# Performance work log

Measured on AMD Instinct MI355X. Metric: run time of the kernel, lower is better.

## Reference

```python
import jax, jax.numpy as jnp
import numpy as np

B, T, C, H = 4, 2048, 1024, 16
D = C // H  # head dim = 64


def setup_inputs() -> dict:
    key = jax.random.key(0)
    ks = jax.random.split(key, 5)
    s = 1.0 / np.sqrt(C)
    return {
        "x": jax.random.normal(ks[0], (B, T, C), jnp.float32),
        "Wq": jax.random.normal(ks[1], (C, C), jnp.float32) * s,
        "bq": jnp.zeros((C,), jnp.float32),
        "Wk": jax.random.normal(ks[2], (C, C), jnp.float32) * s,
        "bk": jnp.zeros((C,), jnp.float32),
        "Wv": jax.random.normal(ks[3], (C, C), jnp.float32) * s,
        "bv": jnp.zeros((C,), jnp.float32),
        "Wp": jax.random.normal(ks[4], (C, C), jnp.float32) * s,
        "bp": jnp.zeros((C,), jnp.float32),
    }


def reference(x, Wq, bq, Wk, bk, Wv, bv, Wp, bp):
    # linear projections -> [B, H, T, D]
    def heads(t):
        return t.reshape(B, T, H, D).transpose(0, 2, 1, 3)
    q = heads(x @ Wq.T + bq)
    k = heads(x @ Wk.T + bk)
    v = heads(x @ Wv.T + bv)
    scale = 1.0 / np.sqrt(D)
    att = jnp.einsum("bhtd,bhsd->bhts", q, k) * scale  # [B,H,T,T]
    causal = jnp.tril(jnp.ones((T, T), bool))
    att = jnp.where(causal[None, None], att, -jnp.inf)
    att = jax.nn.softmax(att, axis=-1)
    y = jnp.einsum("bhts,bhsd->bhtd", att, v)  # [B,H,T,D]
    y = y.transpose(0, 2, 1, 3).reshape(B, T, C)
    return y @ Wp.T + bp
```

## Files before the change

### kernel.cpp

```cpp
#include <hip/hip_runtime.h>

typedef float f32x4 __attribute__((ext_vector_type(4)));
typedef float f32x16 __attribute__((ext_vector_type(16)));
typedef __bf16 bf16x8 __attribute__((ext_vector_type(8)));
typedef unsigned short u16x8 __attribute__((ext_vector_type(8)));
typedef unsigned int u32x4 __attribute__((ext_vector_type(4)));

#define SCQ 0.1803368801111183f

__device__ inline unsigned short f2bf(float f) {
  unsigned int u = __builtin_bit_cast(unsigned int, f);
  u += 0x7FFFu + ((u >> 16) & 1u);
  return (unsigned short)(u >> 16);
}

__device__ inline float fexp2(float x) {
#if __has_builtin(__builtin_amdgcn_exp2f)
  return __builtin_amdgcn_exp2f(x);
#else
  return exp2f(x);
#endif
}

__device__ inline unsigned int cvtpk_bf16(float a, float b) {
  unsigned int r;
  __asm__("v_cvt_pk_bf16_f32 %0, %1, %2" : "=v"(r) : "v"(a), "v"(b));
  return r;
}
__device__ inline void permswap32(unsigned int& a, unsigned int& b) {
  __asm__("v_permlane32_swap_b32 %0, %1" : "+v"(a), "+v"(b));
}

__device__ inline void gload_lds16(const unsigned short* g, unsigned short* l) {
  __builtin_amdgcn_global_load_lds(
      (const __attribute__((address_space(1))) unsigned int*)g,
      (__attribute__((address_space(3))) unsigned int*)l, 16, 0, 0);
}

__global__ void cvt_x(const float* __restrict__ in, unsigned short* __restrict__ out) {
  int i = (blockIdx.x * 256 + threadIdx.x) * 4;
  float4 f = *(const float4*)(in + i);
  ushort4 o;
  o.x = f2bf(f.x); o.y = f2bf(f.y); o.z = f2bf(f.z); o.w = f2bf(f.w);
  *(ushort4*)(out + i) = o;
}

__global__ void cvt_w(const float* __restrict__ a, const float* __restrict__ b,
                      const float* __restrict__ c, const float* __restrict__ d,
                      unsigned short* __restrict__ oa, unsigned short* __restrict__ ob,
                      unsigned short* __restrict__ oc, unsigned short* __restrict__ od) {
  const float* src[4] = {a, b, c, d};
  unsigned short* dst[4] = {oa, ob, oc, od};
  int m = blockIdx.y;
  int i = (blockIdx.x * 256 + threadIdx.x) * 4;
  float4 f = *(const float4*)(src[m] + i);
  ushort4 o;
  o.x = f2bf(f.x); o.y = f2bf(f.y); o.z = f2bf(f.z); o.w = f2bf(f.w);
  *(ushort4*)(dst[m] + i) = o;
}

template <int MODE>
__global__ __launch_bounds__(512, 2) void gemm256(const unsigned short* __restrict__ A,
                                                  const unsigned short* __restrict__ Bt,
                                                  const float* __restrict__ b0,
                                                  const float* __restrict__ b1,
                                                  const float* __restrict__ b2,
                                                  void* __restrict__ out,
                                                  int M, int N, int K) {
  __shared__ __align__(16) unsigned short Lg[2][4][128 * 64];
  const int tid = threadIdx.x;
  const int lane = tid & 63, w = tid >> 6;
  const int qm = w >> 2, qn = w & 3;
  const int l15 = lane & 15, kq = lane >> 4;

  const int nwg = gridDim.x, qx = nwg >> 3;
  const int wg = blockIdx.x;
  const int wgs = (wg & 7) * qx + (wg >> 3);
  const int nbm = M >> 8;
  const int bm = wgs % nbm, bn = wgs / nbm;
  const int m0 = bm * 256, n0 = bn * 256;
  const int NT = K >> 6, NT4 = NT << 2;

  const int row0 = tid >> 3, c0 = (tid & 7) ^ (row0 & 7);
  const int row1 = row0 + 64, c1 = (tid & 7) ^ (row1 & 7);
  const int ch0 = tid, ch1 = tid + 512;

  auto stage = [&](int g) {
    if (g < NT4) {
      const int tt = g >> 2, h = g & 3;
      const unsigned short* s_;
      int rbase, reg_;
      if (h == 0)      { s_ = A;  rbase = m0;       reg_ = 0; }
      else if (h == 3) { s_ = A;  rbase = m0 + 128; reg_ = 1; }
      else if (h == 1) { s_ = Bt; rbase = n0;       reg_ = 2; }
      else             { s_ = Bt; rbase = n0 + 128; reg_ = 3; }
      unsigned short* d = &Lg[tt & 1][reg_][0];
      gload_lds16(s_ + (size_t)(rbase + row0) * K + tt * 64 + c0 * 8, d + ch0 * 8);
      gload_lds16(s_ + (size_t)(rbase + row1) * K + tt * 64 + c1 * 8, d + ch1 * 8);
    }
  };

  auto rdAh = [&](const unsigned short* R, u16x8 (&a)[4][2]) {
#pragma unroll
    for (int mf = 0; mf < 4; mf++) {
      int row = qm * 64 + mf * 16 + l15;
#pragma unroll
      for (int kf = 0; kf < 2; kf++) {
        int pc = (kf * 4 + kq) ^ (row & 7);
        a[mf][kf] = *(const u16x8*)(R + row * 64 + pc * 8);
      }
    }
  };
  auto rdBh = [&](const unsigned short* R, u16x8 (&bb)[2][2]) {
#pragma unroll
    for (int nf = 0; nf < 2; nf++) {
      int row = qn * 32 + nf * 16 + l15;
#pragma unroll
      for (int kf = 0; kf < 2; kf++) {
        int pc = (kf * 4 + kq) ^ (row & 7);
        bb[nf][kf] = *(const u16x8*)(R + row * 64 + pc * 8);
      }
    }
  };
  auto domfma = [&](u16x8 (&a)[4][2], u16x8 (&bb)[2][2], f32x4 (*ac)[2]) {
#pragma unroll
    for (int mf = 0; mf < 4; mf++)
#pragma unroll
      for (int nf = 0; nf < 2; nf++)
#pragma unroll
        for (int kf = 0; kf < 2; kf++)
          ac[mf][nf] = __builtin_amdgcn_mfma_f32_16x16x32_bf16(
              __builtin_bit_cast(bf16x8, a[mf][kf]),
              __builtin_bit_cast(bf16x8, bb[nf][kf]), ac[mf][nf], 0, 0, 0);
  };

  f32x4 acc[4][4][2] = {};

#pragma unroll
  for (int g = 0; g < 7; ++g) stage(g);
  __asm__ __volatile__("s_waitcnt vmcnt(6)" ::: "memory");
  __builtin_amdgcn_s_barrier();

  for (int tt = 0; tt < NT; ++tt) {
    const unsigned short* A0r = &Lg[tt & 1][0][0];
    const unsigned short* A1r = &Lg[tt & 1][1][0];
    const unsigned short* B0r = &Lg[tt & 1][2][0];
    const unsigned short* B1r = &Lg[tt & 1][3][0];
    const int gb = 7 + 4 * tt;
    u16x8 aA[4][2], bb0[2][2], bb1[2][2];

    rdAh(A0r, aA); rdBh(B0r, bb0);
    stage(gb + 0);
    __builtin_amdgcn_s_barrier();
    __asm__ __volatile__("s_waitcnt lgkmcnt(0)" ::: "memory");
    __builtin_amdgcn_sched_barrier(0);
    __builtin_amdgcn_s_setprio(1);
    domfma(aA, bb0, acc[0]);
    __builtin_amdgcn_s_setprio(0);
    __builtin_amdgcn_s_barrier();

    rdBh(B1r, bb1);
    stage(gb + 1);
    __builtin_amdgcn_s_barrier();
    __asm__ __volatile__("s_waitcnt lgkmcnt(0)" ::: "memory");
    __builtin_amdgcn_sched_barrier(0);
    __builtin_amdgcn_s_setprio(1);
    domfma(aA, bb1, acc[1]);
    __builtin_amdgcn_s_setprio(0);
    __builtin_amdgcn_s_barrier();

    rdAh(A1r, aA);
    stage(gb + 2);
    __builtin_amdgcn_s_barrier();
    __asm__ __volatile__("s_waitcnt lgkmcnt(0)" ::: "memory");
    __builtin_amdgcn_sched_barrier(0);
    __builtin_amdgcn_s_setprio(1);
    domfma(aA, bb0, acc[2]);
    __builtin_amdgcn_s_setprio(0);
    __builtin_amdgcn_s_barrier();

    stage(gb + 3);
    __builtin_amdgcn_s_setprio(1);
    domfma(aA, bb1, acc[3]);
    __builtin_amdgcn_s_setprio(0);
    if (tt < NT - 2) {
      __asm__ __volatile__("s_waitcnt vmcnt(6)" ::: "memory");
    } else if (tt == NT - 2) {
      __asm__ __volatile__("s_waitcnt vmcnt(0)" ::: "memory");
    }
    __builtin_amdgcn_s_barrier();
  }

#pragma unroll
  for (int p = 0; p < 4; p++) {
    const int rb = m0 + (p >> 1) * 128 + qm * 64 + kq * 4;
    const int cb = n0 + (p & 1) * 128 + qn * 32 + l15;
#pragma unroll
    for (int nf = 0; nf < 2; nf++) {
      const int col = cb + nf * 16;
      float bv, sc;
      int which = 0, cl = col;
      if (MODE == 0) {
        which = col >> 10; cl = col & 1023;
        const float* bp = (which == 0) ? b0 : ((which == 1) ? b1 : b2);
        bv = bp[cl];
        sc = (which == 0) ? SCQ : 1.f;
      } else {
        bv = b0[col]; sc = 1.f;
      }
#pragma unroll
      for (int mf = 0; mf < 4; mf++) {
        f32x4 v4 = acc[p][mf][nf];
#pragma unroll
        for (int r = 0; r < 4; r++) {
          int row = rb + mf * 16 + r;
          float v = (v4[r] + bv) * sc;
          if (MODE == 0) {
            int h = cl >> 6, d = cl & 63;
            int b = row >> 11, t = row & 2047;
            ((unsigned short*)out)[(size_t)which * 8388608 +
                                   ((size_t)((b * 16 + h) * 2048 + t)) * 64 + d] = f2bf(v);
          } else {
            ((float*)out)[(size_t)row * N + col] = v;
          }
        }
      }
    }
  }
}

__global__ __launch_bounds__(256) void transpose_v(const unsigned short* __restrict__ V,
                                                   unsigned short* __restrict__ Vt) {
  constexpr int P = 66;
  __shared__ unsigned short L[64 * P];
  const int tid = threadIdx.x;
  const int bh = blockIdx.y;
  const int t0 = blockIdx.x * 64;
  const unsigned short* Vp = V + (size_t)bh * 2048 * 64;
  unsigned short* Op = Vt + (size_t)bh * 64 * 2048;
#pragma unroll
  for (int j = 0; j < 2; j++) {
    int r = (tid >> 3) + j * 32;
    int c = (tid & 7) * 8;
    u16x8 v = *(const u16x8*)(Vp + (size_t)(t0 + r) * 64 + c);
#pragma unroll
    for (int i = 0; i < 4; i++) {
      unsigned int pk = (unsigned int)v[2 * i] | ((unsigned int)v[2 * i + 1] << 16);
      *(unsigned int*)&L[r * P + c + 2 * i] = pk;
    }
  }
  __syncthreads();
#pragma unroll
  for (int j = 0; j < 2; j++) {
    int ch = j * 256 + tid;
    int d = ch >> 3, tc = (ch & 7) * 8;
    u16x8 o;
#pragma unroll
    for (int k = 0; k < 8; k++) o[k] = L[(tc + k) * P + d];
    *(u16x8*)(Op + (size_t)d * 2048 + t0 + tc) = o;
  }
}

__global__ __launch_bounds__(256, 2) void attn_kernel(const unsigned short* __restrict__ Q,
                                                      const unsigned short* __restrict__ Km,
                                                      const unsigned short* __restrict__ Vt,
                                                      unsigned short* __restrict__ Y) {
  constexpr int T = 2048, D = 64;
  __shared__ __align__(16) unsigned short Ks[2][64 * 64];
  __shared__ __align__(16) unsigned short Vs[2][64 * 64];
  const int tid = threadIdx.x;
  const int lane = tid & 63, w = tid >> 6;
  const int l31 = lane & 31, half = lane >> 5;
  const int bh = blockIdx.x;
  const int b = bh >> 4, h = bh & 15;
  const int p = blockIdx.y;
  const unsigned short* Qp = Q + (size_t)bh * T * D;
  const unsigned short* Kp = Km + (size_t)bh * T * D;
  const unsigned short* Vp = Vt + (size_t)bh * D * T;

  const int bch0 = (w * 2) * 64, bch1 = (w * 2 + 1) * 64;
  const int ch0 = bch0 + lane, ch1 = bch1 + lane;
  const int row0 = ch0 >> 3, c0 = (ch0 & 7) ^ (row0 & 7);
  const int row1 = ch1 >> 3, c1 = (ch1 & 7) ^ (row1 & 7);

  for (int phase = 0; phase < 2; ++phase) {
    const int jt = phase ? (63 - (p * 4 + w)) : (p * 4 + w);
    const int qt = jt * 32;
    const int nit = phase ? (32 - 2 * p) : (2 * p + 2);
    const int qg = qt + l31;

    bf16x8 aq[4];
#pragma unroll
    for (int kc = 0; kc < 4; kc++)
      aq[kc] = *(const bf16x8*)(Qp + (size_t)qg * D + kc * 16 + half * 8);
    __asm__ __volatile__("" :: "v"(__builtin_bit_cast(f32x4, aq[0])),
                              "v"(__builtin_bit_cast(f32x4, aq[1])),
                              "v"(__builtin_bit_cast(f32x4, aq[2])),
                              "v"(__builtin_bit_cast(f32x4, aq[3])));

    f32x16 o0 = {}, o1 = {};
    float lsum = 0.f;

    gload_lds16(Kp + (size_t)row0 * 64 + c0 * 8, Ks[0] + bch0 * 8);
    gload_lds16(Kp + (size_t)row1 * 64 + c1 * 8, Ks[0] + bch1 * 8);
    gload_lds16(Vp + (size_t)row0 * T + c0 * 8, Vs[0] + bch0 * 8);
    gload_lds16(Vp + (size_t)row1 * T + c1 * 8, Vs[0] + bch1 * 8);

    int cur = 0;
    for (int it = 0; it < nit; ++it) {
      const int s0 = it * 64;
      if (it + 1 < nit) {
        const int s1 = s0 + 64;
        unsigned short* kd = Ks[cur ^ 1];
        unsigned short* vd = Vs[cur ^ 1];
        gload_lds16(Kp + (size_t)(s1 + row0) * 64 + c0 * 8, kd + bch0 * 8);
        gload_lds16(Kp + (size_t)(s1 + row1) * 64 + c1 * 8, kd + bch1 * 8);
        gload_lds16(Vp + (size_t)row0 * T + s1 + c0 * 8, vd + bch0 * 8);
        gload_lds16(Vp + (size_t)row1 * T + s1 + c1 * 8, vd + bch1 * 8);
        __asm__ __volatile__("s_waitcnt vmcnt(4)" ::: "memory");
      } else {
        __asm__ __volatile__("s_waitcnt vmcnt(0)" ::: "memory");
      }
      __builtin_amdgcn_s_barrier();
      __builtin_amdgcn_sched_barrier(0);

      if (s0 <= qt + 31) {
        const unsigned short* Kb_ = Ks[cur];
        const unsigned short* Vb_ = Vs[cur];

        f32x16 sacc0 = {}, sacc1 = {};
#pragma unroll
        for (int kc = 0; kc < 4; kc++) {
          int kr0 = l31;
          int cc0 = (kc * 2 + half) ^ (kr0 & 7);
          u16x8 k0 = *(const u16x8*)(Kb_ + kr0 * 64 + cc0 * 8);
          sacc0 = __builtin_amdgcn_mfma_f32_32x32x16_bf16(
              __builtin_bit_cast(bf16x8, k0), aq[kc], sacc0, 0, 0, 0);
          int kr1 = 32 + l31;
          int cc1 = (kc * 2 + half) ^ (kr1 & 7);
          u16x8 k1 = *(const u16x8*)(Kb_ + kr1 * 64 + cc1 * 8);
          sacc1 = __builtin_amdgcn_mfma_f32_32x32x16_bf16(
              __builtin_bit_cast(bf16x8, k1), aq[kc], sacc1, 0, 0, 0);
        }

        const bool full = (s0 + 63) <= qt;
        float e0_[16], e1_[16];
        if (full) {
#pragma unroll
          for (int r = 0; r < 16; r++) { e0_[r] = fexp2(sacc0[r]); lsum += e0_[r]; }
#pragma unroll
          for (int r = 0; r < 16; r++) { e1_[r] = fexp2(sacc1[r]); lsum += e1_[r]; }
        } else {
#pragma unroll
          for (int r = 0; r < 16; r++) {
            int sg = s0 + (r & 3) + 8 * (r >> 2) + 4 * half;
            float ex = fexp2(sacc0[r]);
            ex = (sg > qg) ? 0.f : ex;
            e0_[r] = ex; lsum += ex;
          }
#pragma unroll
          for (int r = 0; r < 16; r++) {
            int sg = s0 + 32 + (r & 3) + 8 * (r >> 2) + 4 * half;
            float ex = fexp2(sacc1[r]);
            ex = (sg > qg) ? 0.f : ex;
            e1_[r] = ex; lsum += ex;
          }
        }

        bf16x8 pf[4];
        auto pack2 = [&](const float* e_, int kbase) {
#pragma unroll
          for (int kl = 0; kl < 2; kl++) {
            int base = kl * 8;
            unsigned int a0 = cvtpk_bf16(e_[base + 0], e_[base + 1]);
            unsigned int b0v = cvtpk_bf16(e_[base + 4], e_[base + 5]);
            permswap32(a0, b0v);
            unsigned int a1 = cvtpk_bf16(e_[base + 2], e_[base + 3]);
            unsigned int b1v = cvtpk_bf16(e_[base + 6], e_[base + 7]);
            permswap32(a1, b1v);
            u32x4 t = {a0, a1, b0v, b1v};
            pf[kbase + kl] = __builtin_bit_cast(bf16x8, t);
          }
        };
        pack2(e0_, 0);
        pack2(e1_, 2);

#pragma unroll
        for (int kc = 0; kc < 4; kc++) {
          int vr0 = l31;
          int cc0 = (kc * 2 + half) ^ (vr0 & 7);
          u16x8 v0 = *(const u16x8*)(Vb_ + vr0 * 64 + cc0 * 8);
          o0 = __builtin_amdgcn_mfma_f32_32x32x16_bf16(
              __builtin_bit_cast(bf16x8, v0), pf[kc], o0, 0, 0, 0);
          int vr1 = 32 + l31;
          int cc1 = (kc * 2 + half) ^ (vr1 & 7);
          u16x8 v1 = *(const u16x8*)(Vb_ + vr1 * 64 + cc1 * 8);
          o1 = __builtin_amdgcn_mfma_f32_32x32x16_bf16(
              __builtin_bit_cast(bf16x8, v1), pf[kc], o1, 0, 0, 0);
        }
      }

      __builtin_amdgcn_sched_barrier(0);
      __builtin_amdgcn_s_barrier();
      cur ^= 1;
    }

    float tot = lsum + __shfl_xor(lsum, 32);
    float inv = 1.f / tot;
    unsigned short* Yrow = Y + ((size_t)(b * T + qg)) * 1024 + h * 64;
#pragma unroll
    for (int rp = 0; rp < 8; rp++) {
      int r = rp * 2;
      int d = (r & 3) + 8 * (r >> 2) + 4 * half;
      *(unsigned int*)(Yrow + d)      = cvtpk_bf16(o0[r] * inv, o0[r + 1] * inv);
      *(unsigned int*)(Yrow + 32 + d) = cvtpk_bf16(o1[r] * inv, o1[r + 1] * inv);
    }
  }
}

extern "C" void kernel_launch(void* const* d_in, const int* in_sizes, int n_in,
                              void* d_out, int out_size, void* d_ws, size_t ws_size,
                              hipStream_t stream) {
  const float* x  = (const float*)d_in[0];
  const float* Wq = (const float*)d_in[1];
  const float* bq = (const float*)d_in[2];
  const float* Wk = (const float*)d_in[3];
  const float* bk = (const float*)d_in[4];
  const float* Wv = (const float*)d_in[5];
  const float* bv = (const float*)d_in[6];
  const float* Wp = (const float*)d_in[7];
  const float* bp = (const float*)d_in[8];

  char* ws = (char*)d_ws;
  unsigned short* xb  = (unsigned short*)(ws + 0);
  unsigned short* wqb = (unsigned short*)(ws + 16777216);
  unsigned short* wkb = (unsigned short*)(ws + 18874368);
  unsigned short* wvb = (unsigned short*)(ws + 20971520);
  unsigned short* wpb = (unsigned short*)(ws + 23068672);
  unsigned short* Qb  = (unsigned short*)(ws + 25165824);
  unsigned short* Kb  = (unsigned short*)(ws + 41943040);
  unsigned short* Vb  = (unsigned short*)(ws + 58720256);
  unsigned short* Vtb = xb;
  unsigned short* Yb  = Vb;

  cvt_x<<<8192, 256, 0, stream>>>(x, xb);
  cvt_w<<<dim3(1024, 4), 256, 0, stream>>>(Wq, Wk, Wv, Wp, wqb, wkb, wvb, wpb);

  gemm256<0><<<384, 512, 0, stream>>>(xb, wqb, bq, bk, bv, Qb, 8192, 3072, 1024);

  transpose_v<<<dim3(32, 64), 256, 0, stream>>>(Vb, Vtb);
  attn_kernel<<<dim3(64, 8), 256, 0, stream>>>(Qb, Kb, Vtb, Yb);

  gemm256<1><<<128, 512, 0, stream>>>(Yb, wpb, bp, bp, bp, d_out, 8192, 1024, 1024);
}
```

Baseline: 265.5 us.

## Shrink GEMM tile to 128x256 with two-phase pipeline and simple grid mapping

The 256x256 GEMM tile with a four-phase LDS pipeline becomes a 128x256 tile: one A half and two B halves per k-step, three LDS regions per buffer, and two MFMA phases per iteration. The grid doubles (768 and 256 blocks) and the swizzled 1D block mapping is replaced by a plain 2D grid. The aim is to fill more CUs, since the old 128-block output GEMM left many of them idle, and to reduce LDS use. The cost is lower arithmetic intensity per tile, and dropping the swizzle may hurt L2 locality.

Result: faster. 248.5 us (-6.4%).

```diff
diff --git a/kernel.cpp b/kernel.cpp
--- a/kernel.cpp
+++ b/kernel.cpp
@@ -60,47 +60,35 @@
 }
 
 template <int MODE>
-__global__ __launch_bounds__(512, 2) void gemm256(const unsigned short* __restrict__ A,
-                                                  const unsigned short* __restrict__ Bt,
-                                                  const float* __restrict__ b0,
-                                                  const float* __restrict__ b1,
-                                                  const float* __restrict__ b2,
-                                                  void* __restrict__ out,
-                                                  int M, int N, int K) {
-  __shared__ __align__(16) unsigned short Lg[2][4][128 * 64];
+__global__ __launch_bounds__(512, 2) void gemm8p(const unsigned short* __restrict__ A,
+                                                 const unsigned short* __restrict__ Bt,
+                                                 const float* __restrict__ b0,
+                                                 const float* __restrict__ b1,
+                                                 const float* __restrict__ b2,
+                                                 void* __restrict__ out,
+                                                 int M, int N, int K) {
+  __shared__ __align__(16) unsigned short Lg[2][3][128 * 64];
   const int tid = threadIdx.x;
   const int lane = tid & 63, w = tid >> 6;
   const int qm = w >> 2, qn = w & 3;
   const int l15 = lane & 15, kq = lane >> 4;
-
-  const int nwg = gridDim.x, qx = nwg >> 3;
-  const int wg = blockIdx.x;
-  const int wgs = (wg & 7) * qx + (wg >> 3);
-  const int nbm = M >> 8;
-  const int bm = wgs % nbm, bn = wgs / nbm;
-  const int m0 = bm * 256, n0 = bn * 256;
-  const int NT = K >> 6, NT4 = NT << 2;
+  const int m0 = blockIdx.x * 128, n0 = blockIdx.y * 256;
+  const int NT = K >> 6;
 
   const int row0 = tid >> 3, c0 = (tid & 7) ^ (row0 & 7);
   const int row1 = row0 + 64, c1 = (tid & 7) ^ (row1 & 7);
-  const int ch0 = tid, ch1 = tid + 512;
-
-  auto stage = [&](int g) {
-    if (g < NT4) {
-      const int tt = g >> 2, h = g & 3;
-      const unsigned short* s_;
-      int rbase, reg_;
-      if (h == 0)      { s_ = A;  rbase = m0;       reg_ = 0; }
-      else if (h == 3) { s_ = A;  rbase = m0 + 128; reg_ = 1; }
-      else if (h == 1) { s_ = Bt; rbase = n0;       reg_ = 2; }
-      else             { s_ = Bt; rbase = n0 + 128; reg_ = 3; }
-      unsigned short* d = &Lg[tt & 1][reg_][0];
-      gload_lds16(s_ + (size_t)(rbase + row0) * K + tt * 64 + c0 * 8, d + ch0 * 8);
-      gload_lds16(s_ + (size_t)(rbase + row1) * K + tt * 64 + c1 * 8, d + ch1 * 8);
+
+  auto stage = [&](int tt, int h) {
+    if (tt < NT) {
+      const unsigned short* s_ = (h == 0) ? A : Bt;
+      const int rbase = (h == 0) ? m0 : (h == 1 ? n0 : n0 + 128);
+      unsigned short* d = &Lg[tt & 1][h][0];
+      gload_lds16(s_ + (size_t)(rbase + row0) * K + tt * 64 + c0 * 8, d + (size_t)tid * 8);
+      gload_lds16(s_ + (size_t)(rbase + row1) * K + tt * 64 + c1 * 8, d + (size_t)(tid + 512) * 8);
     }
   };
 
-  auto rdAh = [&](const unsigned short* R, u16x8 (&a)[4][2]) {
+  auto rdA = [&](const unsigned short* R, u16x8 (&a)[4][2]) {
 #pragma unroll
     for (int mf = 0; mf < 4; mf++) {
       int row = qm * 64 + mf * 16 + l15;
@@ -111,7 +99,7 @@
       }
     }
   };
-  auto rdBh = [&](const unsigned short* R, u16x8 (&bb)[2][2]) {
+  auto rdB = [&](const unsigned short* R, u16x8 (&bb)[2][2]) {
 #pragma unroll
     for (int nf = 0; nf < 2; nf++) {
       int row = qn * 32 + nf * 16 + l15;
@@ -122,69 +110,51 @@
       }
     }
   };
-  auto domfma = [&](u16x8 (&a)[4][2], u16x8 (&bb)[2][2], f32x4 (*ac)[2]) {
+
+  f32x4 acc[4][4] = {};
+
+  auto domfma = [&](u16x8 (&a)[4][2], u16x8 (&bb)[2][2], int hb) {
 #pragma unroll
     for (int mf = 0; mf < 4; mf++)
 #pragma unroll
       for (int nf = 0; nf < 2; nf++)
 #pragma unroll
         for (int kf = 0; kf < 2; kf++)
-          ac[mf][nf] = __builtin_amdgcn_mfma_f32_16x16x32_bf16(
+          acc[mf][hb * 2 + nf] = __builtin_amdgcn_mfma_f32_16x16x32_bf16(
               __builtin_bit_cast(bf16x8, a[mf][kf]),
-              __builtin_bit_cast(bf16x8, bb[nf][kf]), ac[mf][nf], 0, 0, 0);
+              __builtin_bit_cast(bf16x8, bb[nf][kf]), acc[mf][hb * 2 + nf], 0, 0, 0);
   };
 
-  f32x4 acc[4][4][2] = {};
-
-#pragma unroll
-  for (int g = 0; g < 7; ++g) stage(g);
-  __asm__ __volatile__("s_waitcnt vmcnt(6)" ::: "memory");
+  stage(0, 0); stage(0, 1); stage(0, 2); stage(1, 0); stage(1, 1);
+  __asm__ __volatile__("s_waitcnt vmcnt(4)" ::: "memory");
   __builtin_amdgcn_s_barrier();
 
   for (int tt = 0; tt < NT; ++tt) {
-    const unsigned short* A0r = &Lg[tt & 1][0][0];
-    const unsigned short* A1r = &Lg[tt & 1][1][0];
-    const unsigned short* B0r = &Lg[tt & 1][2][0];
-    const unsigned short* B1r = &Lg[tt & 1][3][0];
-    const int gb = 7 + 4 * tt;
-    u16x8 aA[4][2], bb0[2][2], bb1[2][2];
-
-    rdAh(A0r, aA); rdBh(B0r, bb0);
-    stage(gb + 0);
+    const unsigned short* Ar  = &Lg[tt & 1][0][0];
+    const unsigned short* B0r = &Lg[tt & 1][1][0];
+    const unsigned short* B1r = &Lg[tt & 1][2][0];
+    u16x8 aA[4][2], bb[2][2];
+
+    rdA(Ar, aA); rdB(B0r, bb);
+    stage(tt + 1, 2);
     __builtin_amdgcn_s_barrier();
     __asm__ __volatile__("s_waitcnt lgkmcnt(0)" ::: "memory");
     __builtin_amdgcn_sched_barrier(0);
     __builtin_amdgcn_s_setprio(1);
-    domfma(aA, bb0, acc[0]);
+    domfma(aA, bb, 0);
     __builtin_amdgcn_s_setprio(0);
     __builtin_amdgcn_s_barrier();
 
-    rdBh(B1r, bb1);
-    stage(gb + 1);
+    rdB(B1r, bb);
+    stage(tt + 2, 0); stage(tt + 2, 1);
     __builtin_amdgcn_s_barrier();
     __asm__ __volatile__("s_waitcnt lgkmcnt(0)" ::: "memory");
     __builtin_amdgcn_sched_barrier(0);
     __builtin_amdgcn_s_setprio(1);
-    domfma(aA, bb1, acc[1]);
-    __builtin_amdgcn_s_setprio(0);
-    __builtin_amdgcn_s_barrier();
-
-    rdAh(A1r, aA);
-    stage(gb + 2);
-    __builtin_amdgcn_s_barrier();
-    __asm__ __volatile__("s_waitcnt lgkmcnt(0)" ::: "memory");
-    __builtin_amdgcn_sched_barrier(0);
-    __builtin_amdgcn_s_setprio(1);
-    domfma(aA, bb0, acc[2]);
-    __builtin_amdgcn_s_setprio(0);
-    __builtin_amdgcn_s_barrier();
-
-    stage(gb + 3);
-    __builtin_amdgcn_s_setprio(1);
-    domfma(aA, bb1, acc[3]);
+    domfma(aA, bb, 1);
     __builtin_amdgcn_s_setprio(0);
     if (tt < NT - 2) {
-      __asm__ __volatile__("s_waitcnt vmcnt(6)" ::: "memory");
+      __asm__ __volatile__("s_waitcnt vmcnt(4)" ::: "memory");
     } else if (tt == NT - 2) {
       __asm__ __volatile__("s_waitcnt vmcnt(0)" ::: "memory");
     }
@@ -192,37 +162,32 @@
   }
 
 #pragma unroll
-  for (int p = 0; p < 4; p++) {
-    const int rb = m0 + (p >> 1) * 128 + qm * 64 + kq * 4;
-    const int cb = n0 + (p & 1) * 128 + qn * 32 + l15;
-#pragma unroll
-    for (int nf = 0; nf < 2; nf++) {
-      const int col = cb + nf * 16;
-      float bv, sc;
-      int which = 0, cl = col;
-      if (MODE == 0) {
-        which = col >> 10; cl = col & 1023;
-        const float* bp = (which == 0) ? b0 : ((which == 1) ? b1 : b2);
-        bv = bp[cl];
-        sc = (which == 0) ? SCQ : 1.f;
-      } else {
-        bv = b0[col]; sc = 1.f;
-      }
-#pragma unroll
-      for (int mf = 0; mf < 4; mf++) {
-        f32x4 v4 = acc[p][mf][nf];
-#pragma unroll
-        for (int r = 0; r < 4; r++) {
-          int row = rb + mf * 16 + r;
-          float v = (v4[r] + bv) * sc;
-          if (MODE == 0) {
-            int h = cl >> 6, d = cl & 63;
-            int b = row >> 11, t = row & 2047;
-            ((unsigned short*)out)[(size_t)which * 8388608 +
-                                   ((size_t)((b * 16 + h) * 2048 + t)) * 64 + d] = f2bf(v);
-          } else {
-            ((float*)out)[(size_t)row * N + col] = v;
-          }
+  for (int nfg = 0; nfg < 4; nfg++) {
+    const int col = n0 + (nfg >> 1) * 128 + qn * 32 + (nfg & 1) * 16 + l15;
+    float bv, sc;
+    int which = 0, cl = col;
+    if (MODE == 0) {
+      which = col >> 10; cl = col & 1023;
+      const float* bp = (which == 0) ? b0 : ((which == 1) ? b1 : b2);
+      bv = bp[cl];
+      sc = (which == 0) ? SCQ : 1.f;
+    } else {
+      bv = b0[col]; sc = 1.f;
+    }
+#pragma unroll
+    for (int mf = 0; mf < 4; mf++) {
+      f32x4 v4 = acc[mf][nfg];
+#pragma unroll
+      for (int r = 0; r < 4; r++) {
+        int row = m0 + qm * 64 + mf * 16 + kq * 4 + r;
+        float v = (v4[r] + bv) * sc;
+        if (MODE == 0) {
+          int h = cl >> 6, d = cl & 63;
+          int b = row >> 11, t = row & 2047;
+          ((unsigned short*)out)[(size_t)which * 8388608 +
+                                 ((size_t)((b * 16 + h) * 2048 + t)) * 64 + d] = f2bf(v);
+        } else {
+          ((float*)out)[(size_t)row * N + col] = v;
         }
       }
     }
@@ -446,10 +411,10 @@
   cvt_x<<<8192, 256, 0, stream>>>(x, xb);
   cvt_w<<<dim3(1024, 4), 256, 0, stream>>>(Wq, Wk, Wv, Wp, wqb, wkb, wvb, wpb);
 
-  gemm256<0><<<384, 512, 0, stream>>>(xb, wqb, bq, bk, bv, Qb, 8192, 3072, 1024);
+  gemm8p<0><<<dim3(64, 12), 512, 0, stream>>>(xb, wqb, bq, bk, bv, Qb, 8192, 3072, 1024);
 
   transpose_v<<<dim3(32, 64), 256, 0, stream>>>(Vb, Vtb);
   attn_kernel<<<dim3(64, 8), 256, 0, stream>>>(Qb, Kb, Vtb, Yb);
 
-  gemm256<1><<<128, 512, 0, stream>>>(Yb, wpb, bp, bp, bp, d_out, 8192, 1024, 1024);
-}
+  gemm8p<1><<<dim3(64, 4), 512, 0, stream>>>(Yb, wpb, bp, bp, bp, d_out, 8192, 1024, 1024);
+}
```
